# Optimization experiments

Measured on AMD Instinct MI355X. Metric: run time of the kernel, lower is better.

The kernel has to match this reference:

```python
import jax, jax.numpy as jnp
import numpy as np

N, E, G, NP = 65536, 524288, 256, 256
C, L, H, DH = 256, 4, 4, 64
IN_DIM, E_DIM = 771, 4
LN_EPS = 1e-5


def _ln(h, g, b):
    mu = jnp.mean(h, -1, keepdims=True)
    v = jnp.mean((h - mu) ** 2, -1, keepdims=True)
    return (h - mu) * jax.lax.rsqrt(v + LN_EPS) * g + b


def _bn(h, g, b):
    mu = jnp.mean(h, 0)
    v = jnp.mean((h - mu) ** 2, 0)
    return (h - mu) * jax.lax.rsqrt(v + LN_EPS) * g + b


def setup_inputs() -> dict:
    key = jax.random.key(0)
    ks = iter(jax.random.split(key, 64))
    def rn(shape, s=0.02):
        return jax.random.normal(next(ks), shape, jnp.float32) * s
    inp = {}
    inp["x"] = jax.random.normal(next(ks), (N, IN_DIM), jnp.float32)
    src = jax.random.randint(next(ks), (E,), 0, N, jnp.int32)
    dst = jax.random.randint(next(ks), (E,), 0, N, jnp.int32)
    inp["edge_index"] = jnp.stack([src, dst])
    inp["batch"] = jnp.arange(N, dtype=jnp.int32) // NP  # 256 graphs of 256 nodes
    inp["edge_attr"] = jax.random.normal(next(ks), (E, E_DIM), jnp.float32)
    # encoders
    inp["ne_w"] = rn((IN_DIM, C)); inp["ne_b"] = jnp.zeros((C,), jnp.float32)
    inp["ne_ln_g"] = jnp.ones((C,), jnp.float32); inp["ne_ln_b"] = jnp.zeros((C,), jnp.float32)
    inp["ee_w"] = rn((E_DIM, C)); inp["ee_b"] = jnp.zeros((C,), jnp.float32)
    # per-layer stacked params
    inp["eps"] = jnp.zeros((L,), jnp.float32)
    for nm, shape in [("elin_w", (L, C, C)), ("gin_w1", (L, C, C)), ("gin_w2", (L, C, C)),
                      ("attn_in_w", (L, 3 * C, C)), ("attn_out_w", (L, C, C)),
                      ("mlp_w1", (L, C, 2 * C)), ("mlp_w2", (L, 2 * C, C))]:
        inp[nm] = rn(shape)
    for nm, shape in [("elin_b", (L, C)), ("gin_b1", (L, C)), ("gin_b2", (L, C)),
                      ("attn_in_b", (L, 3 * C)), ("attn_out_b", (L, C)),
                      ("mlp_b1", (L, 2 * C)), ("mlp_b2", (L, C))]:
        inp[nm] = jnp.zeros(shape, jnp.float32)
    for nm in ["gin_bn_g", "ln1_g", "ln2_g", "ln3_g"]:
        inp[nm] = jnp.ones((L, C), jnp.float32)
    for nm in ["gin_bn_b", "ln1_b", "ln2_b", "ln3_b"]:
        inp[nm] = jnp.zeros((L, C), jnp.float32)
    inp["cls_w1"] = rn((C, C)); inp["cls_b1"] = jnp.zeros((C,), jnp.float32)
    inp["cls_ln_g"] = jnp.ones((C,), jnp.float32); inp["cls_ln_b"] = jnp.zeros((C,), jnp.float32)
    inp["cls_w2"] = rn((C, C // 2)); inp["cls_b2"] = jnp.zeros((C // 2,), jnp.float32)
    inp["cls_w3"] = rn((C // 2, 1)); inp["cls_b3"] = jnp.zeros((1,), jnp.float32)
    return inp


def _forward(edge_index, batch, x, edge_attr, ne_w, ne_b, ne_ln_g, ne_ln_b, ee_w, ee_b,
             eps, elin_w, elin_b, gin_w1, gin_b1, gin_bn_g, gin_bn_b, gin_w2, gin_b2,
             attn_in_w, attn_in_b, attn_out_w, attn_out_b,
             ln1_g, ln1_b, ln2_g, ln2_b, ln3_g, ln3_b,
             mlp_w1, mlp_b1, mlp_w2, mlp_b2,
             cls_w1, cls_b1, cls_ln_g, cls_ln_b, cls_w2, cls_b2, cls_w3, cls_b3):
    src, dst = edge_index[0], edge_index[1]
    # node / edge encoders (dropout = identity, eval mode)
    h = jax.nn.relu(_ln(x @ ne_w + ne_b, ne_ln_g, ne_ln_b))
    e = jax.nn.relu(edge_attr @ ee_w + ee_b)  # [E, C]
    scale = DH ** -0.5
    for l in range(L):
        # --- GINEConv: msg = relu(x_j + lin(edge_attr)), sum-aggregate at dst ---
        ee = e @ elin_w[l] + elin_b[l]
        msg = jax.nn.relu(h[src] + ee)                              # [E, C] gather
        aggr = jax.ops.segment_sum(msg, dst, num_segments=N)        # [N, C] scatter
        g1 = (1.0 + eps[l]) * h + aggr
        g1 = jax.nn.relu(_bn(g1 @ gin_w1[l] + gin_b1[l], gin_bn_g[l], gin_bn_b[l]))
        h_local = g1 @ gin_w2[l] + gin_b2[l]
        h_local = _ln(h_local + h, ln1_g[l], ln1_b[l])
        # --- global multi-head attention over dense-batched graphs ---
        hd = h.reshape(G, NP, C)
        qkv = hd @ attn_in_w[l].T + attn_in_b[l]                    # [G, NP, 3C]
        q, k, v = jnp.split(qkv, 3, axis=-1)
        q = q.reshape(G, NP, H, DH)
        k = k.reshape(G, NP, H, DH)
        v = v.reshape(G, NP, H, DH)
        scores = jnp.einsum('bqhd,bkhd->bhqk', q, k) * scale
        a = jax.nn.softmax(scores, axis=-1)
        o = jnp.einsum('bhqk,bkhd->bqhd', a, v).reshape(G, NP, C)
        o = (o @ attn_out_w[l].T + attn_out_b[l]).reshape(N, C)
        h_attn = _ln(o + h, ln2_g[l], ln2_b[l])
        # --- combine + FFN + final norm ---
        out = h_local + h_attn
        m = jax.nn.relu(out @ mlp_w1[l] + mlp_b1[l]) @ mlp_w2[l] + mlp_b2[l]
        h = _ln(out + m, ln3_g[l], ln3_b[l])
    # global mean pool per graph
    sums = jax.ops.segment_sum(h, batch, num_segments=G)
    cnt = jax.ops.segment_sum(jnp.ones((N, 1), h.dtype), batch, num_segments=G)
    gemb = sums / jnp.maximum(cnt, 1.0)
    z = jax.nn.relu(_ln(gemb @ cls_w1 + cls_b1, cls_ln_g, cls_ln_b))
    z = jax.nn.relu(z @ cls_w2 + cls_b2)
    return (z @ cls_w3 + cls_b3)[:, 0]


def reference(x, edge_index, batch, edge_attr, ne_w, ne_b, ne_ln_g, ne_ln_b, ee_w, ee_b,
              eps, elin_w, elin_b, gin_w1, gin_b1, gin_bn_g, gin_bn_b, gin_w2, gin_b2,
              attn_in_w, attn_in_b, attn_out_w, attn_out_b,
              ln1_g, ln1_b, ln2_g, ln2_b, ln3_g, ln3_b,
              mlp_w1, mlp_b1, mlp_w2, mlp_b2,
              cls_w1, cls_b1, cls_ln_g, cls_ln_b, cls_w2, cls_b2, cls_w3, cls_b3):
    return _forward(edge_index, batch, x, edge_attr, ne_w, ne_b, ne_ln_g, ne_ln_b, ee_w, ee_b,
                    eps, elin_w, elin_b, gin_w1, gin_b1, gin_bn_g, gin_bn_b, gin_w2, gin_b2,
                    attn_in_w, attn_in_b, attn_out_w, attn_out_b,
                    ln1_g, ln1_b, ln2_g, ln2_b, ln3_g, ln3_b,
                    mlp_w1, mlp_b1, mlp_w2, mlp_b2,
                    cls_w1, cls_b1, cls_ln_g, cls_ln_b, cls_w2, cls_b2, cls_w3, cls_b3)
```

## Files before the change

kernel.cpp:

```cpp
#include <hip/hip_runtime.h>
#include <hip/hip_bf16.h>
#include <math.h>

#define N_NODES 65536
#define N_EDGES 524288
#define CH 256

#define FMA4(A4, S, W4) \
  A4.x = fmaf((S), (W4).x, A4.x); A4.y = fmaf((S), (W4).y, A4.y); \
  A4.z = fmaf((S), (W4).z, A4.z); A4.w = fmaf((S), (W4).w, A4.w)

typedef __bf16 bf16x8 __attribute__((ext_vector_type(8)));
typedef float f32x4 __attribute__((ext_vector_type(4)));

__device__ inline unsigned short bf16rn(float v) {
  unsigned int u = __float_as_uint(v);
  u = u + 0x7FFFu + ((u >> 16) & 1u);
  return (unsigned short)(u >> 16);
}

__device__ inline bf16x8 pack_bf16_8(const float4 a, const float4 b) {
  union { __hip_bfloat162 h2[4]; bf16x8 v; } r;
  r.h2[0] = __float22bfloat162_rn(make_float2(a.x, a.y));
  r.h2[1] = __float22bfloat162_rn(make_float2(a.z, a.w));
  r.h2[2] = __float22bfloat162_rn(make_float2(b.x, b.y));
  r.h2[3] = __float22bfloat162_rn(make_float2(b.z, b.w));
  return r.v;
}

__global__ __launch_bounds__(256) void wcvt_kernel(
    const float* __restrict__ W, unsigned short* __restrict__ P,
    int K, int Nn, int transposed)
{
  const int idx = blockIdx.x * 256 + threadIdx.x;
  const int k = idx / Nn;
  const int n = idx - k * Nn;
  const float v = transposed ? W[(size_t)n * K + k] : W[(size_t)k * Nn + n];
  P[(((size_t)(k >> 3)) * Nn + n) * 8 + (k & 7)] = bf16rn(v);
}

__global__ __launch_bounds__(256) void xcvt_kernel(
    const float* __restrict__ x, unsigned short* __restrict__ xs)
{
  const int t = blockIdx.x * 256 + threadIdx.x;
  const int row = t / 98;
  const int c = t - row * 98;
  const int k0 = c << 3;
  unsigned short hi[8], lo[8];
#pragma unroll
  for (int j = 0; j < 8; ++j) {
    const int k = k0 + j;
    const float v = (k < 771) ? x[(size_t)row * 771 + k] : 0.f;
    const unsigned short h16 = bf16rn(v);
    const float hf = __uint_as_float(((unsigned int)h16) << 16);
    hi[j] = h16;
    lo[j] = bf16rn(v - hf);
  }
  unsigned short* base = xs + (size_t)row * 1568 + k0;
  *(uint4*)base = *(const uint4*)hi;
  *(uint4*)(base + 784) = *(const uint4*)lo;
}

template <bool RELU, bool ABF16>
__global__ __launch_bounds__(256, 3) void mgemm_kernel(
    const void* __restrict__ Av, const unsigned short* __restrict__ Bp,
    const float* __restrict__ bias, float* __restrict__ Cmat,
    int M, int Nn, int K)
{
  const int tid = threadIdx.x;
  const int lane = tid & 63;
  const int w = tid >> 6;
  const int m_base = blockIdx.y * 64;
  const int n_base = blockIdx.x * 256 + w * 64;
  const int lr = lane & 15;
  const int lq = lane >> 4;
  f32x4 acc[4][4];
#pragma unroll
  for (int i = 0; i < 4; ++i)
#pragma unroll
    for (int j = 0; j < 4; ++j) acc[i][j] = (f32x4){0.f, 0.f, 0.f, 0.f};

  for (int k0 = 0; k0 < K; k0 += 32) {
    const int ka = k0 + (lq << 3);
    bf16x8 af[4], bfv[4];
#pragma unroll
    for (int mt = 0; mt < 4; ++mt) {
      if (ABF16) {
        const unsigned short* ap =
            (const unsigned short*)Av + (size_t)(m_base + mt * 16 + lr) * K + ka;
        union { uint4 u; bf16x8 b; } au;
        au.u = *(const uint4*)ap;
        af[mt] = au.b;
      } else {
        const float* ap = (const float*)Av + (size_t)(m_base + mt * 16 + lr) * K + ka;
        af[mt] = pack_bf16_8(*(const float4*)ap, *(const float4*)(ap + 4));
      }
    }
#pragma unroll
    for (int nt = 0; nt < 4; ++nt) {
      const size_t off =
          (((size_t)(ka >> 3)) * Nn + (n_base + nt * 16 + lr)) << 3;
      union { uint4 u; bf16x8 b; } bu;
      bu.u = *(const uint4*)(Bp + off);
      bfv[nt] = bu.b;
    }
#pragma unroll
    for (int mt = 0; mt < 4; ++mt)
#pragma unroll
      for (int nt = 0; nt < 4; ++nt)
        acc[mt][nt] = __builtin_amdgcn_mfma_f32_16x16x32_bf16(
            af[mt], bfv[nt], acc[mt][nt], 0, 0, 0);
  }
#pragma unroll
  for (int nt = 0; nt < 4; ++nt) {
    const int col = n_base + nt * 16 + lr;
    const float bv = bias[col];
#pragma unroll
    for (int mt = 0; mt < 4; ++mt) {
      const int row0 = m_base + mt * 16 + (lq << 2);
#pragma unroll
      for (int r = 0; r < 4; ++r) {
        float v = acc[mt][nt][r] + bv;
        if (RELU) v = fmaxf(v, 0.f);
        Cmat[(size_t)(row0 + r) * Nn + col] = v;
      }
    }
  }
}

__global__ __launch_bounds__(256, 3) void eegemm_kernel(
    const float* __restrict__ edge_attr,
    const int* __restrict__ eid_sorted,
    const int* __restrict__ row_ptr, int node_base,
    const float* __restrict__ ee_w, const float* __restrict__ ee_b,
    const unsigned short* __restrict__ elin_p, const float* __restrict__ elin_b,
    float* __restrict__ EE)
{
  __shared__ float wenc[4][256];
  __shared__ float benc[256];
  const int tid = threadIdx.x;
  const int slot_base = row_ptr[node_base];
  const int slot_end = row_ptr[node_base + 16384];
  const int m_rel = blockIdx.y * 128;
  if (slot_base + m_rel >= slot_end) return;

  ((float4*)wenc)[tid] = ((const float4*)ee_w)[tid];
  if (tid < 64) ((float4*)benc)[tid] = ((const float4*)ee_b)[tid];
  __syncthreads();

  const int lane = tid & 63;
  const int w = tid >> 6;
  const int m_base = m_rel + (w >> 1) * 64;
  const int n_base = blockIdx.x * 128 + (w & 1) * 64;
  const int lr = lane & 15;
  const int lq = lane >> 4;

  float4 ea_r[4];
#pragma unroll
  for (int mt = 0; mt < 4; ++mt) {
    const int abs_slot = slot_base + m_base + mt * 16 + lr;
    if (abs_slot < slot_end) {
      const int e = eid_sorted[abs_slot];
      ea_r[mt] = *(const float4*)(edge_attr + ((size_t)e << 2));
    } else {
      ea_r[mt] = make_float4(0.f, 0.f, 0.f, 0.f);
    }
  }

  f32x4 acc[4][4];
#pragma unroll
  for (int i = 0; i < 4; ++i)
#pragma unroll
    for (int j = 0; j < 4; ++j) acc[i][j] = (f32x4){0.f, 0.f, 0.f, 0.f};

  for (int k0 = 0; k0 < 256; k0 += 32) {
    const int ka = k0 + (lq << 3);
    const float4 b0 = *(const float4*)&benc[ka];
    const float4 b1 = *(const float4*)&benc[ka + 4];
    float4 w0[4], w1[4];
#pragma unroll
    for (int j = 0; j < 4; ++j) {
      w0[j] = *(const float4*)&wenc[j][ka];
      w1[j] = *(const float4*)&wenc[j][ka + 4];
    }
    bf16x8 af[4], bfv[4];
#pragma unroll
    for (int mt = 0; mt < 4; ++mt) {
      float4 v0 = b0, v1 = b1;
      FMA4(v0, ea_r[mt].x, w0[0]); FMA4(v1, ea_r[mt].x, w1[0]);
      FMA4(v0, ea_r[mt].y, w0[1]); FMA4(v1, ea_r[mt].y, w1[1]);
      FMA4(v0, ea_r[mt].z, w0[2]); FMA4(v1, ea_r[mt].z, w1[2]);
      FMA4(v0, ea_r[mt].w, w0[3]); FMA4(v1, ea_r[mt].w, w1[3]);
      v0.x = fmaxf(v0.x, 0.f); v0.y = fmaxf(v0.y, 0.f);
      v0.z = fmaxf(v0.z, 0.f); v0.w = fmaxf(v0.w, 0.f);
      v1.x = fmaxf(v1.x, 0.f); v1.y = fmaxf(v1.y, 0.f);
      v1.z = fmaxf(v1.z, 0.f); v1.w = fmaxf(v1.w, 0.f);
      af[mt] = pack_bf16_8(v0, v1);
    }
#pragma unroll
    for (int nt = 0; nt < 4; ++nt) {
      const size_t off =
          (((size_t)(ka >> 3)) * 256 + (n_base + nt * 16 + lr)) << 3;
      union { uint4 u; bf16x8 b; } bu;
      bu.u = *(const uint4*)(elin_p + off);
      bfv[nt] = bu.b;
    }
#pragma unroll
    for (int mt = 0; mt < 4; ++mt)
#pragma unroll
      for (int nt = 0; nt < 4; ++nt)
        acc[mt][nt] = __builtin_amdgcn_mfma_f32_16x16x32_bf16(
            af[mt], bfv[nt], acc[mt][nt], 0, 0, 0);
  }

#pragma unroll
  for (int nt = 0; nt < 4; ++nt) {
    const int col = n_base + nt * 16 + lr;
    const float bv = elin_b[col];
#pragma unroll
    for (int mt = 0; mt < 4; ++mt) {
      const int row0 = m_base + mt * 16 + (lq << 2);
#pragma unroll
      for (int r = 0; r < 4; ++r) {
        if (slot_base + row0 + r < slot_end)
          EE[(size_t)(row0 + r) * 256 + col] = acc[mt][nt][r] + bv;
      }
    }
  }
}

__global__ __launch_bounds__(256, 8) void gscat2_kernel(
    const float* __restrict__ EE,
    const int* __restrict__ src_sorted,
    const int* __restrict__ row_ptr, int node_base,
    const float* __restrict__ h, const float* __restrict__ eps, int layer,
    float* __restrict__ g1)
{
  const int tid = threadIdx.x;
  const int w = tid >> 6;
  const int lane = tid & 63;
  const int n = node_base + (blockIdx.x << 2) + w;
  const int cg = lane << 2;
  const int slot_base = row_ptr[node_base];
  const int row_start = row_ptr[n];
  const int row_end = row_ptr[n + 1];

  float4 acc0 = make_float4(0.f, 0.f, 0.f, 0.f);
  float4 acc1 = make_float4(0.f, 0.f, 0.f, 0.f);
  int slot = row_start;
  for (; slot + 2 <= row_end; slot += 2) {
    const int s0 = src_sorted[slot];
    const int s1 = src_sorted[slot + 1];
    const float4 e0 = *(const float4*)(EE + (size_t)(slot - slot_base) * 256 + cg);
    const float4 e1 = *(const float4*)(EE + (size_t)(slot + 1 - slot_base) * 256 + cg);
    const float4 h0 = *(const float4*)(h + (((size_t)s0) << 8) + cg);
    const float4 h1 = *(const float4*)(h + (((size_t)s1) << 8) + cg);
    acc0.x += fmaxf(h0.x + e0.x, 0.f);
    acc0.y += fmaxf(h0.y + e0.y, 0.f);
    acc0.z += fmaxf(h0.z + e0.z, 0.f);
    acc0.w += fmaxf(h0.w + e0.w, 0.f);
    acc1.x += fmaxf(h1.x + e1.x, 0.f);
    acc1.y += fmaxf(h1.y + e1.y, 0.f);
    acc1.z += fmaxf(h1.z + e1.z, 0.f);
    acc1.w += fmaxf(h1.w + e1.w, 0.f);
  }
  if (slot < row_end) {
    const int s0 = src_sorted[slot];
    const float4 e0 = *(const float4*)(EE + (size_t)(slot - slot_base) * 256 + cg);
    const float4 h0 = *(const float4*)(h + (((size_t)s0) << 8) + cg);
    acc0.x += fmaxf(h0.x + e0.x, 0.f);
    acc0.y += fmaxf(h0.y + e0.y, 0.f);
    acc0.z += fmaxf(h0.z + e0.z, 0.f);
    acc0.w += fmaxf(h0.w + e0.w, 0.f);
  }
  acc0.x += acc1.x; acc0.y += acc1.y; acc0.z += acc1.z; acc0.w += acc1.w;

  const float f = 1.f + eps[layer];
  const float4 hv = *(const float4*)(h + (((size_t)n) << 8) + cg);
  float4 o;
  o.x = fmaf(f, hv.x, acc0.x);
  o.y = fmaf(f, hv.y, acc0.y);
  o.z = fmaf(f, hv.z, acc0.z);
  o.w = fmaf(f, hv.w, acc0.w);
  *(float4*)(g1 + (((size_t)n) << 8) + cg) = o;
}

template <bool BT, bool RELU>
__global__ __launch_bounds__(256, 4) void gemm_kernel(
    const float* __restrict__ A, const float* __restrict__ B,
    const float* __restrict__ bias, float* __restrict__ Cmat,
    int M, int Nn, int K)
{
  __shared__ float As[8][132];
  __shared__ float Bs[8][132];
  const int tid = threadIdx.x;
  const int bm = blockIdx.y * 128;
  const int bn = blockIdx.x * 128;
  const int tm = (tid >> 4) << 3;
  const int tn = (tid & 15) << 3;
  float acc[8][8];
#pragma unroll
  for (int i = 0; i < 8; ++i)
#pragma unroll
    for (int j = 0; j < 8; ++j) acc[i][j] = 0.f;

  const int nk = (K + 7) >> 3;
  const bool k4 = (K & 3) == 0;
  for (int kc = 0; kc < nk; ++kc) {
    const int k0 = kc << 3;
    {
      const int r = tid >> 1;
      const int kk = (tid & 1) << 2;
      const int gm = bm + r;
      float va[4] = {0.f, 0.f, 0.f, 0.f};
      if (gm < M) {
        const size_t base = (size_t)gm * K + k0 + kk;
        if (k4 && (k0 + kk + 4 <= K)) {
          const float4 v = *(const float4*)(A + base);
          va[0] = v.x; va[1] = v.y; va[2] = v.z; va[3] = v.w;
        } else {
#pragma unroll
          for (int j = 0; j < 4; ++j)
            if (k0 + kk + j < K) va[j] = A[base + j];
        }
      }
      As[kk + 0][r] = va[0]; As[kk + 1][r] = va[1];
      As[kk + 2][r] = va[2]; As[kk + 3][r] = va[3];
    }
    if (!BT) {
      const int r = tid >> 5;
      const int cb = (tid & 31) << 2;
      float4 v = make_float4(0.f, 0.f, 0.f, 0.f);
      if (k0 + r < K) v = *(const float4*)(B + (size_t)(k0 + r) * Nn + bn + cb);
      *(float4*)&Bs[r][cb] = v;
    } else {
      const int r = tid >> 1;
      const int kk = (tid & 1) << 2;
      float vb[4] = {0.f, 0.f, 0.f, 0.f};
      if (bn + r < Nn) {
        const size_t base = (size_t)(bn + r) * K + k0 + kk;
        if (k4 && (k0 + kk + 4 <= K)) {
          const float4 v = *(const float4*)(B + base);
          vb[0] = v.x; vb[1] = v.y; vb[2] = v.z; vb[3] = v.w;
        } else {
#pragma unroll
          for (int j = 0; j < 4; ++j)
            if (k0 + kk + j < K) vb[j] = B[base + j];
        }
      }
      Bs[kk + 0][r] = vb[0]; Bs[kk + 1][r] = vb[1];
      Bs[kk + 2][r] = vb[2]; Bs[kk + 3][r] = vb[3];
    }
    __syncthreads();
#pragma unroll
    for (int k = 0; k < 8; ++k) {
      const float4 a0 = *(const float4*)&As[k][tm];
      const float4 a1 = *(const float4*)&As[k][tm + 4];
      const float4 b0 = *(const float4*)&Bs[k][tn];
      const float4 b1 = *(const float4*)&Bs[k][tn + 4];
      const float av[8] = {a0.x, a0.y, a0.z, a0.w, a1.x, a1.y, a1.z, a1.w};
      const float bv[8] = {b0.x, b0.y, b0.z, b0.w, b1.x, b1.y, b1.z, b1.w};
#pragma unroll
      for (int i = 0; i < 8; ++i)
#pragma unroll
        for (int j = 0; j < 8; ++j)
          acc[i][j] = fmaf(av[i], bv[j], acc[i][j]);
    }
    __syncthreads();
  }
#pragma unroll
  for (int i = 0; i < 8; ++i) {
    const int gm = bm + tm + i;
    if (gm >= M) continue;
    float* crow = Cmat + (size_t)gm * Nn + bn + tn;
#pragma unroll
    for (int j = 0; j < 8; ++j) {
      const int gn = bn + tn + j;
      if (gn >= Nn) continue;
      float v = acc[i][j] + (bias ? bias[gn] : 0.f);
      if (RELU) v = fmaxf(v, 0.f);
      crow[j] = v;
    }
  }
}

__global__ __launch_bounds__(256) void hist_kernel(
    const int* __restrict__ dst, int* __restrict__ deg)
{
  const int e = blockIdx.x * 256 + threadIdx.x;
  atomicAdd(&deg[dst[e]], 1);
}

__global__ __launch_bounds__(256) void scan_kernel(
    const int* __restrict__ deg, int* __restrict__ row_ptr,
    int* __restrict__ fill)
{
  __shared__ int part[256];
  const int t = threadIdx.x;
  const int base = t << 8;
  int s = 0;
  for (int j = 0; j < 256; ++j) s += deg[base + j];
  part[t] = s;
  __syncthreads();
  for (int off = 1; off < 256; off <<= 1) {
    int v = (t >= off) ? part[t - off] : 0;
    __syncthreads();
    part[t] += v;
    __syncthreads();
  }
  int run = (t == 0) ? 0 : part[t - 1];
  for (int j = 0; j < 256; ++j) {
    row_ptr[base + j] = run;
    fill[base + j] = run;
    run += deg[base + j];
  }
  if (t == 255) row_ptr[65536] = run;
}

__global__ __launch_bounds__(256) void scatter_kernel(
    const int* __restrict__ dst, const int* __restrict__ src,
    int* __restrict__ fill, int* __restrict__ eid, int* __restrict__ ssrc)
{
  const int e = blockIdx.x * 256 + threadIdx.x;
  const int pos = atomicAdd(&fill[dst[e]], 1);
  eid[pos] = e;
  ssrc[pos] = src[e];
}

__global__ __launch_bounds__(256, 1) void mattn_kernel(
    const float* __restrict__ qkv, float* __restrict__ o)
{
  __shared__ __attribute__((aligned(16))) unsigned short Ks[256 * 72];
  __shared__ __attribute__((aligned(16))) unsigned short Vt[64 * 258];
  __shared__ __attribute__((aligned(16))) unsigned short Ps[4][64 * 72];
  const int tid = threadIdx.x;
  const int gh = blockIdx.x;
  const int g = gh >> 2;
  const int hh = gh & 3;
  const int lane = tid & 63;
  const int w = tid >> 6;
  const int lr = lane & 15;
  const int lq = lane >> 4;
  const float scale = 0.125f;

  {
    const int key0 = tid >> 4;
    const int c0 = (tid & 15) << 2;
#pragma unroll
    for (int it = 0; it < 16; ++it) {
      const int key = it * 16 + key0;
      const float* base = qkv + ((size_t)(g * 256 + key)) * 768 + hh * 64 + c0;
      const float4 kv = *(const float4*)(base + 256);
      const float4 vv = *(const float4*)(base + 512);
      union { __hip_bfloat162 h2[2]; ushort4 u; } pk;
      pk.h2[0] = __float22bfloat162_rn(make_float2(kv.x, kv.y));
      pk.h2[1] = __float22bfloat162_rn(make_float2(kv.z, kv.w));
      *(ushort4*)&Ks[key * 72 + c0] = pk.u;
      Vt[(c0 + 0) * 258 + key] = bf16rn(vv.x);
      Vt[(c0 + 1) * 258 + key] = bf16rn(vv.y);
      Vt[(c0 + 2) * 258 + key] = bf16rn(vv.z);
      Vt[(c0 + 3) * 258 + key] = bf16rn(vv.w);
    }
  }

  const int m0 = w * 64;
  bf16x8 qf[2][4];
#pragma unroll
  for (int ks = 0; ks < 2; ++ks)
#pragma unroll
    for (int mt = 0; mt < 4; ++mt) {
      const float* ap = qkv +
          ((size_t)(g * 256 + m0 + mt * 16 + lr)) * 768 + hh * 64 +
          ks * 32 + (lq << 3);
      float4 a = *(const float4*)ap;
      float4 b = *(const float4*)(ap + 4);
      a.x *= scale; a.y *= scale; a.z *= scale; a.w *= scale;
      b.x *= scale; b.y *= scale; b.z *= scale; b.w *= scale;
      qf[ks][mt] = pack_bf16_8(a, b);
    }
  __syncthreads();

  f32x4 oacc[4][4];
#pragma unroll
  for (int i = 0; i < 4; ++i)
#pragma unroll
    for (int j = 0; j < 4; ++j) oacc[i][j] = (f32x4){0.f, 0.f, 0.f, 0.f};
  float lpart[4][4];
#pragma unroll
  for (int i = 0; i < 4; ++i)
#pragma unroll
    for (int j = 0; j < 4; ++j) lpart[i][j] = 0.f;

  unsigned short* Pw = Ps[w];

  for (int kb = 0; kb < 4; ++kb) {
    f32x4 sacc[4][4];
#pragma unroll
    for (int i = 0; i < 4; ++i)
#pragma unroll
      for (int j = 0; j < 4; ++j) sacc[i][j] = (f32x4){0.f, 0.f, 0.f, 0.f};
#pragma unroll
    for (int ks = 0; ks < 2; ++ks) {
      bf16x8 bfv[4];
#pragma unroll
      for (int nt = 0; nt < 4; ++nt) {
        union { uint4 u; bf16x8 b; } bu;
        bu.u = *(const uint4*)&Ks[(kb * 64 + nt * 16 + lr) * 72 +
                                  ks * 32 + (lq << 3)];
        bfv[nt] = bu.b;
      }
#pragma unroll
      for (int mt = 0; mt < 4; ++mt)
#pragma unroll
        for (int nt = 0; nt < 4; ++nt)
          sacc[mt][nt] = __builtin_amdgcn_mfma_f32_16x16x32_bf16(
              qf[ks][mt], bfv[nt], sacc[mt][nt], 0, 0, 0);
    }
#pragma unroll
    for (int mt = 0; mt < 4; ++mt)
#pragma unroll
      for (int nt = 0; nt < 4; ++nt) {
#pragma unroll
        for (int rr = 0; rr < 4; ++rr) {
          const float p = __expf(sacc[mt][nt][rr]);
          lpart[mt][rr] += p;
          Pw[(mt * 16 + (lq << 2) + rr) * 72 + nt * 16 + lr] = bf16rn(p);
        }
      }
    asm volatile("s_waitcnt lgkmcnt(0)" ::: "memory");
    __builtin_amdgcn_sched_barrier(0);
#pragma unroll
    for (int ks = 0; ks < 2; ++ks) {
      bf16x8 pa[4], vb[4];
#pragma unroll
      for (int mt = 0; mt < 4; ++mt) {
        union { uint4 u; bf16x8 b; } au;
        au.u = *(const uint4*)&Pw[(mt * 16 + lr) * 72 + ks * 32 + (lq << 3)];
        pa[mt] = au.b;
      }
#pragma unroll
      for (int nt = 0; nt < 4; ++nt) {
        const unsigned short* vp =
            &Vt[(nt * 16 + lr) * 258 + kb * 64 + ks * 32 + (lq << 3)];
        union { unsigned int u4[4]; bf16x8 b; } vu;
        vu.u4[0] = *(const unsigned int*)(vp + 0);
        vu.u4[1] = *(const unsigned int*)(vp + 2);
        vu.u4[2] = *(const unsigned int*)(vp + 4);
        vu.u4[3] = *(const unsigned int*)(vp + 6);
        vb[nt] = vu.b;
      }
#pragma unroll
      for (int mt = 0; mt < 4; ++mt)
#pragma unroll
        for (int nt = 0; nt < 4; ++nt)
          oacc[mt][nt] = __builtin_amdgcn_mfma_f32_16x16x32_bf16(
              pa[mt], vb[nt], oacc[mt][nt], 0, 0, 0);
    }
  }

#pragma unroll
  for (int mt = 0; mt < 4; ++mt)
#pragma unroll
    for (int rr = 0; rr < 4; ++rr) {
      float v = lpart[mt][rr];
      v += __shfl_xor(v, 1);
      v += __shfl_xor(v, 2);
      v += __shfl_xor(v, 4);
      v += __shfl_xor(v, 8);
      lpart[mt][rr] = 1.f / v;
    }

#pragma unroll
  for (int mt = 0; mt < 4; ++mt) {
#pragma unroll
    for (int nt = 0; nt < 4; ++nt) {
#pragma unroll
      for (int rr = 0; rr < 4; ++rr) {
        const int row = m0 + mt * 16 + (lq << 2) + rr;
        o[((size_t)(g * 256 + row)) * 256 + hh * 64 + nt * 16 + lr] =
            oacc[mt][nt][rr] * lpart[mt][rr];
      }
    }
  }
}

__global__ __launch_bounds__(256) void ln_kernel(
    const float* __restrict__ a, const float* __restrict__ res,
    const float* __restrict__ gam, const float* __restrict__ bet,
    float* __restrict__ out, int relu)
{
  __shared__ float2 red[256];
  const int t = threadIdx.x;
  const size_t base = (size_t)blockIdx.x * 256;
  float v = a[base + t];
  if (res) v += res[base + t];
  red[t] = make_float2(v, v * v);
  __syncthreads();
#pragma unroll
  for (int s = 128; s > 0; s >>= 1) {
    if (t < s) { red[t].x += red[t + s].x; red[t].y += red[t + s].y; }
    __syncthreads();
  }
  const float mu = red[0].x * (1.f / 256.f);
  const float var = red[0].y * (1.f / 256.f) - mu * mu;
  float r = (v - mu) * rsqrtf(var + 1e-5f) * gam[t] + bet[t];
  if (relu) r = fmaxf(r, 0.f);
  out[base + t] = r;
}

__global__ __launch_bounds__(256) void bn_stats_kernel(
    const float* __restrict__ y, float* __restrict__ stats)
{
  const int t = threadIdx.x;
  const size_t r0 = (size_t)blockIdx.x * 64;
  float s = 0.f, s2 = 0.f;
  for (int r = 0; r < 64; ++r) {
    const float v = y[(r0 + r) * 256 + t];
    s += v;
    s2 = fmaf(v, v, s2);
  }
  atomicAdd(&stats[t], s);
  atomicAdd(&stats[256 + t], s2);
}

__global__ __launch_bounds__(256) void bn_apply_kernel(
    float* __restrict__ y, const float* __restrict__ stats,
    const float* __restrict__ gam, const float* __restrict__ bet)
{
  const size_t i = ((size_t)blockIdx.x * 256 + threadIdx.x) << 2;
  const int c = (int)(i & 255);
  const float inv_n = 1.f / 65536.f;
  float4 v = *(float4*)(y + i);
  const float4 s4 = *(const float4*)(stats + c);
  const float4 q4 = *(const float4*)(stats + 256 + c);
  const float4 g4 = *(const float4*)(gam + c);
  const float4 b4 = *(const float4*)(bet + c);
  float mu, var, sc;
  mu = s4.x * inv_n; var = q4.x * inv_n - mu * mu; sc = g4.x * rsqrtf(var + 1e-5f);
  v.x = fmaxf((v.x - mu) * sc + b4.x, 0.f);
  mu = s4.y * inv_n; var = q4.y * inv_n - mu * mu; sc = g4.y * rsqrtf(var + 1e-5f);
  v.y = fmaxf((v.y - mu) * sc + b4.y, 0.f);
  mu = s4.z * inv_n; var = q4.z * inv_n - mu * mu; sc = g4.z * rsqrtf(var + 1e-5f);
  v.z = fmaxf((v.z - mu) * sc + b4.z, 0.f);
  mu = s4.w * inv_n; var = q4.w * inv_n - mu * mu; sc = g4.w * rsqrtf(var + 1e-5f);
  v.w = fmaxf((v.w - mu) * sc + b4.w, 0.f);
  *(float4*)(y + i) = v;
}

__global__ __launch_bounds__(256) void add_kernel(
    const float* __restrict__ a, const float* __restrict__ b,
    float* __restrict__ out)
{
  const size_t i = ((size_t)blockIdx.x * 256 + threadIdx.x) << 2;
  const float4 va = *(const float4*)(a + i);
  const float4 vb = *(const float4*)(b + i);
  float4 v;
  v.x = va.x + vb.x; v.y = va.y + vb.y; v.z = va.z + vb.z; v.w = va.w + vb.w;
  *(float4*)(out + i) = v;
}

__global__ __launch_bounds__(256) void pool_kernel(
    const float* __restrict__ h, const int* __restrict__ batch,
    float* __restrict__ sums, float* __restrict__ cnt)
{
  const int t = threadIdx.x;
  const int n0 = blockIdx.x * 256;
  float acc = 0.f, runc = 0.f;
  int cur = batch[n0];
  for (int r = 0; r < 256; ++r) {
    const int n = n0 + r;
    const int b = batch[n];
    if (b != cur) {
      atomicAdd(&sums[(size_t)cur * 256 + t], acc);
      if (t == 0) atomicAdd(&cnt[cur], runc);
      acc = 0.f; runc = 0.f; cur = b;
    }
    acc += h[(size_t)n * 256 + t];
    runc += 1.f;
  }
  atomicAdd(&sums[(size_t)cur * 256 + t], acc);
  if (t == 0) atomicAdd(&cnt[cur], runc);
}

__global__ __launch_bounds__(256) void gemb_kernel(
    const float* __restrict__ sums, const float* __restrict__ cnt,
    float* __restrict__ gemb)
{
  const int i = blockIdx.x * 256 + threadIdx.x;
  const int g = i >> 8;
  gemb[i] = sums[i] / fmaxf(cnt[g], 1.f);
}

__global__ __launch_bounds__(256) void head_kernel(
    const float* __restrict__ z2, const float* __restrict__ w3,
    const float* __restrict__ b3, float* __restrict__ out)
{
  __shared__ float w[128];
  const int t = threadIdx.x;
  if (t < 128) w[t] = w3[t];
  __syncthreads();
  float s = 0.f;
  const float* row = z2 + (size_t)t * 128;
#pragma unroll 4
  for (int d = 0; d < 128; ++d) s = fmaf(row[d], w[d], s);
  out[t] = s + b3[0];
}

extern "C" void kernel_launch(void* const* d_in, const int* in_sizes, int n_in,
                              void* d_out, int out_size, void* d_ws, size_t ws_size,
                              hipStream_t stream)
{
  const float* x          = (const float*)d_in[0];
  const int*   edge_index = (const int*)d_in[1];
  const int*   batch      = (const int*)d_in[2];
  const float* edge_attr  = (const float*)d_in[3];
  const float* ne_w   = (const float*)d_in[4];
  const float* ne_b   = (const float*)d_in[5];
  const float* ne_ln_g = (const float*)d_in[6];
  const float* ne_ln_b = (const float*)d_in[7];
  const float* ee_w   = (const float*)d_in[8];
  const float* ee_b   = (const float*)d_in[9];
  const float* eps    = (const float*)d_in[10];
  const float* elin_w = (const float*)d_in[11];
  const float* gin_w1 = (const float*)d_in[12];
  const float* gin_w2 = (const float*)d_in[13];
  const float* attn_in_w  = (const float*)d_in[14];
  const float* attn_out_w = (const float*)d_in[15];
  const float* mlp_w1 = (const float*)d_in[16];
  const float* mlp_w2 = (const float*)d_in[17];
  const float* elin_b = (const float*)d_in[18];
  const float* gin_b1 = (const float*)d_in[19];
  const float* gin_b2 = (const float*)d_in[20];
  const float* attn_in_b  = (const float*)d_in[21];
  const float* attn_out_b = (const float*)d_in[22];
  const float* mlp_b1 = (const float*)d_in[23];
  const float* mlp_b2 = (const float*)d_in[24];
  const float* gin_bn_g = (const float*)d_in[25];
  const float* ln1_g  = (const float*)d_in[26];
  const float* ln2_g  = (const float*)d_in[27];
  const float* ln3_g  = (const float*)d_in[28];
  const float* gin_bn_b = (const float*)d_in[29];
  const float* ln1_b  = (const float*)d_in[30];
  const float* ln2_b  = (const float*)d_in[31];
  const float* ln3_b  = (const float*)d_in[32];
  const float* cls_w1 = (const float*)d_in[33];
  const float* cls_b1 = (const float*)d_in[34];
  const float* cls_ln_g = (const float*)d_in[35];
  const float* cls_ln_b = (const float*)d_in[36];
  const float* cls_w2 = (const float*)d_in[37];
  const float* cls_b2 = (const float*)d_in[38];
  const float* cls_w3 = (const float*)d_in[39];
  const float* cls_b3 = (const float*)d_in[40];

  const int* src = edge_index;
  const int* dst = edge_index + N_EDGES;

  float* ws = (float*)d_ws;
  const size_t NC = (size_t)N_NODES * CH;
  float* h    = ws;
  float* bufA = ws + NC;
  float* bufB = ws + 2 * NC;
  float* bufC = ws + 3 * NC;
  float* bufQ = ws + 4 * NC;
  float* stats = bufQ + (size_t)N_NODES * 768;
  int* ideg  = (int*)(stats + 2048);
  int* ifill = ideg + 65536;
  int* irow  = ifill + 65536;
  int* ieid  = irow + 65544;
  int* issrc = ieid + 524288;
  unsigned short* pan = (unsigned short*)(issrc + 524288);
  unsigned short* xs = (unsigned short*)bufC;
  float* sums = bufA;
  float* cnt  = bufA + 65536;
  float* gemb = bufA + 65792;
  float* z1   = bufA + 131328;
  float* z2   = bufA + 196864;

  const dim3 blk(256);
  const size_t PL = 720896;
  unsigned short* panNE = pan + 4 * PL;

  hipMemsetAsync(stats, 0, 2048 * sizeof(float), stream);
  hipMemsetAsync(ideg, 0, 65536 * sizeof(int), stream);
  hipMemsetAsync(panNE, 0, 401408 * sizeof(unsigned short), stream);
  hist_kernel<<<dim3(2048), blk, 0, stream>>>(dst, ideg);
  scan_kernel<<<dim3(1), blk, 0, stream>>>(ideg, irow, ifill);
  scatter_kernel<<<dim3(2048), blk, 0, stream>>>(dst, src, ifill, ieid, issrc);
  for (int l = 0; l < 4; ++l) {
    unsigned short* p = pan + l * PL;
    wcvt_kernel<<<dim3(256), blk, 0, stream>>>(gin_w1 + (size_t)l * 65536, p, 256, 256, 0);
    wcvt_kernel<<<dim3(256), blk, 0, stream>>>(gin_w2 + (size_t)l * 65536, p + 65536, 256, 256, 0);
    wcvt_kernel<<<dim3(768), blk, 0, stream>>>(attn_in_w + (size_t)l * 196608, p + 131072, 256, 768, 1);
    wcvt_kernel<<<dim3(256), blk, 0, stream>>>(attn_out_w + (size_t)l * 65536, p + 327680, 256, 256, 1);
    wcvt_kernel<<<dim3(512), blk, 0, stream>>>(mlp_w1 + (size_t)l * 131072, p + 393216, 256, 512, 0);
    wcvt_kernel<<<dim3(512), blk, 0, stream>>>(mlp_w2 + (size_t)l * 131072, p + 524288, 512, 256, 0);
    wcvt_kernel<<<dim3(256), blk, 0, stream>>>(elin_w + (size_t)l * 65536, p + 655360, 256, 256, 0);
  }
  wcvt_kernel<<<dim3(771), blk, 0, stream>>>(ne_w, panNE, 771, 256, 0);
  wcvt_kernel<<<dim3(771), blk, 0, stream>>>(ne_w, panNE + (size_t)98 * 256 * 8, 771, 256, 0);

  xcvt_kernel<<<dim3(25088), blk, 0, stream>>>(x, xs);
  mgemm_kernel<false, true><<<dim3(1, 1024), blk, 0, stream>>>(
      xs, panNE, ne_b, bufB, N_NODES, 256, 1568);
  ln_kernel<<<dim3(N_NODES), blk, 0, stream>>>(bufB, nullptr, ne_ln_g, ne_ln_b, h, 1);

  for (int l = 0; l < 4; ++l) {
    unsigned short* p = pan + l * PL;
    for (int q = 0; q < 4; ++q) {
      eegemm_kernel<<<dim3(2, 1056), blk, 0, stream>>>(
          edge_attr, ieid, irow, q * 16384, ee_w, ee_b,
          p + 655360, elin_b + l * 256, bufQ);
      gscat2_kernel<<<dim3(4096), blk, 0, stream>>>(
          bufQ, issrc, irow, q * 16384, h, eps, l, bufA);
    }
    mgemm_kernel<false, false><<<dim3(1, 1024), blk, 0, stream>>>(
        bufA, p, gin_b1 + l * 256, bufB, N_NODES, 256, 256);
    bn_stats_kernel<<<dim3(1024), blk, 0, stream>>>(bufB, stats + l * 512);
    bn_apply_kernel<<<dim3(16384), blk, 0, stream>>>(
        bufB, stats + l * 512, gin_bn_g + l * 256, gin_bn_b + l * 256);
    mgemm_kernel<false, false><<<dim3(1, 1024), blk, 0, stream>>>(
        bufB, p + 65536, gin_b2 + l * 256, bufC, N_NODES, 256, 256);
    ln_kernel<<<dim3(N_NODES), blk, 0, stream>>>(
        bufC, h, ln1_g + l * 256, ln1_b + l * 256, bufC, 0);
    mgemm_kernel<false, false><<<dim3(3, 1024), blk, 0, stream>>>(
        h, p + 131072, attn_in_b + l * 768, bufQ, N_NODES, 768, 256);
    mattn_kernel<<<dim3(1024), blk, 0, stream>>>(bufQ, bufA);
    mgemm_kernel<false, false><<<dim3(1, 1024), blk, 0, stream>>>(
        bufA, p + 327680, attn_out_b + l * 256, bufB, N_NODES, 256, 256);
    ln_kernel<<<dim3(N_NODES), blk, 0, stream>>>(
        bufB, h, ln2_g + l * 256, ln2_b + l * 256, bufB, 0);
    add_kernel<<<dim3(16384), blk, 0, stream>>>(bufC, bufB, bufB);
    mgemm_kernel<true, false><<<dim3(2, 1024), blk, 0, stream>>>(
        bufB, p + 393216, mlp_b1 + l * 512, bufQ, N_NODES, 512, 256);
    mgemm_kernel<false, false><<<dim3(1, 1024), blk, 0, stream>>>(
        bufQ, p + 524288, mlp_b2 + l * 256, bufC, N_NODES, 256, 512);
    ln_kernel<<<dim3(N_NODES), blk, 0, stream>>>(
        bufC, bufB, ln3_g + l * 256, ln3_b + l * 256, h, 0);
  }

  hipMemsetAsync(sums, 0, 65792 * sizeof(float), stream);
  pool_kernel<<<dim3(256), blk, 0, stream>>>(h, batch, sums, cnt);
  gemb_kernel<<<dim3(256), blk, 0, stream>>>(sums, cnt, gemb);
  gemm_kernel<false, false><<<dim3(2, 2), blk, 0, stream>>>(
      gemb, cls_w1, cls_b1, z1, 256, 256, 256);
  ln_kernel<<<dim3(256), blk, 0, stream>>>(z1, nullptr, cls_ln_g, cls_ln_b, z1, 1);
  gemm_kernel<false, true><<<dim3(1, 2), blk, 0, stream>>>(
      z1, cls_w2, cls_b2, z2, 256, 128, 256);
  head_kernel<<<dim3(1), blk, 0, stream>>>(z2, cls_w3, cls_b3, (float*)d_out);
}
```

Measured before the change: 6.040 ms.

## Store intermediate activations in bf16 to halve memory traffic across kernels

Producers (eegemm, gscat, bn_apply, add, LN, QKV and MLP1 GEMMs, attention output) now write bf16 copies of their outputs, and the matrix-core GEMMs and attention read these directly instead of converting fp32 inputs. This cuts bytes moved through HBM for the edge-embedding buffer, gather output, QKV and MLP hidden activations. The attention scale moves from Q to the exponent argument. The cost is extra rounding of intermediates, which may raise numerical error, and some LN/add kernels now do a second store.

```diff
diff --git a/kernel.cpp b/kernel.cpp
--- a/kernel.cpp
+++ b/kernel.cpp
@@ -17,6 +17,17 @@
   unsigned int u = __float_as_uint(v);
   u = u + 0x7FFFu + ((u >> 16) & 1u);
   return (unsigned short)(u >> 16);
+}
+
+__device__ inline float bf2f(unsigned short u) {
+  return __uint_as_float(((unsigned int)u) << 16);
+}
+
+__device__ inline ushort4 pack_bf16_4(const float4 a) {
+  ushort4 r;
+  r.x = bf16rn(a.x); r.y = bf16rn(a.y);
+  r.z = bf16rn(a.z); r.w = bf16rn(a.w);
+  return r;
 }
 
 __device__ inline bf16x8 pack_bf16_8(const float4 a, const float4 b) {
@@ -61,10 +72,10 @@
   *(uint4*)(base + 784) = *(const uint4*)lo;
 }
 
-template <bool RELU, bool ABF16>
+template <bool RELU, bool ABF16, bool CBF16>
 __global__ __launch_bounds__(256, 3) void mgemm_kernel(
     const void* __restrict__ Av, const unsigned short* __restrict__ Bp,
-    const float* __restrict__ bias, float* __restrict__ Cmat,
+    const float* __restrict__ bias, void* __restrict__ Cv,
     int M, int Nn, int K)
 {
   const int tid = threadIdx.x;
@@ -122,7 +133,10 @@
       for (int r = 0; r < 4; ++r) {
         float v = acc[mt][nt][r] + bv;
         if (RELU) v = fmaxf(v, 0.f);
-        Cmat[(size_t)(row0 + r) * Nn + col] = v;
+        if (CBF16)
+          ((unsigned short*)Cv)[(size_t)(row0 + r) * Nn + col] = bf16rn(v);
+        else
+          ((float*)Cv)[(size_t)(row0 + r) * Nn + col] = v;
       }
     }
   }
@@ -134,7 +148,7 @@
     const int* __restrict__ row_ptr, int node_base,
     const float* __restrict__ ee_w, const float* __restrict__ ee_b,
     const unsigned short* __restrict__ elin_p, const float* __restrict__ elin_b,
-    float* __restrict__ EE)
+    unsigned short* __restrict__ EE)
 {
   __shared__ float wenc[4][256];
   __shared__ float benc[256];
@@ -223,18 +237,18 @@
 #pragma unroll
       for (int r = 0; r < 4; ++r) {
         if (slot_base + row0 + r < slot_end)
-          EE[(size_t)(row0 + r) * 256 + col] = acc[mt][nt][r] + bv;
+          EE[(size_t)(row0 + r) * 256 + col] = bf16rn(acc[mt][nt][r] + bv);
       }
     }
   }
 }
 
 __global__ __launch_bounds__(256, 8) void gscat2_kernel(
-    const float* __restrict__ EE,
+    const unsigned short* __restrict__ EE,
     const int* __restrict__ src_sorted,
     const int* __restrict__ row_ptr, int node_base,
     const float* __restrict__ h, const float* __restrict__ eps, int layer,
-    float* __restrict__ g1)
+    unsigned short* __restrict__ g1b)
 {
   const int tid = threadIdx.x;
   const int w = tid >> 6;
@@ -251,27 +265,27 @@
   for (; slot + 2 <= row_end; slot += 2) {
     const int s0 = src_sorted[slot];
     const int s1 = src_sorted[slot + 1];
-    const float4 e0 = *(const float4*)(EE + (size_t)(slot - slot_base) * 256 + cg);
-    const float4 e1 = *(const float4*)(EE + (size_t)(slot + 1 - slot_base) * 256 + cg);
+    const ushort4 eu0 = *(const ushort4*)(EE + (size_t)(slot - slot_base) * 256 + cg);
+    const ushort4 eu1 = *(const ushort4*)(EE + (size_t)(slot + 1 - slot_base) * 256 + cg);
     const float4 h0 = *(const float4*)(h + (((size_t)s0) << 8) + cg);
     const float4 h1 = *(const float4*)(h + (((size_t)s1) << 8) + cg);
-    acc0.x += fmaxf(h0.x + e0.x, 0.f);
-    acc0.y += fmaxf(h0.y + e0.y, 0.f);
-    acc0.z += fmaxf(h0.z + e0.z, 0.f);
-    acc0.w += fmaxf(h0.w + e0.w, 0.f);
-    acc1.x += fmaxf(h1.x + e1.x, 0.f);
-    acc1.y += fmaxf(h1.y + e1.y, 0.f);
-    acc1.z += fmaxf(h1.z + e1.z, 0.f);
-    acc1.w += fmaxf(h1.w + e1.w, 0.f);
+    acc0.x += fmaxf(h0.x + bf2f(eu0.x), 0.f);
+    acc0.y += fmaxf(h0.y + bf2f(eu0.y), 0.f);
+    acc0.z += fmaxf(h0.z + bf2f(eu0.z), 0.f);
+    acc0.w += fmaxf(h0.w + bf2f(eu0.w), 0.f);
+    acc1.x += fmaxf(h1.x + bf2f(eu1.x), 0.f);
+    acc1.y += fmaxf(h1.y + bf2f(eu1.y), 0.f);
+    acc1.z += fmaxf(h1.z + bf2f(eu1.z), 0.f);
+    acc1.w += fmaxf(h1.w + bf2f(eu1.w), 0.f);
   }
   if (slot < row_end) {
     const int s0 = src_sorted[slot];
-    const float4 e0 = *(const float4*)(EE + (size_t)(slot - slot_base) * 256 + cg);
+    const ushort4 eu0 = *(const ushort4*)(EE + (size_t)(slot - slot_base) * 256 + cg);
     const float4 h0 = *(const float4*)(h + (((size_t)s0) << 8) + cg);
-    acc0.x += fmaxf(h0.x + e0.x, 0.f);
-    acc0.y += fmaxf(h0.y + e0.y, 0.f);
-    acc0.z += fmaxf(h0.z + e0.z, 0.f);
-    acc0.w += fmaxf(h0.w + e0.w, 0.f);
+    acc0.x += fmaxf(h0.x + bf2f(eu0.x), 0.f);
+    acc0.y += fmaxf(h0.y + bf2f(eu0.y), 0.f);
+    acc0.z += fmaxf(h0.z + bf2f(eu0.z), 0.f);
+    acc0.w += fmaxf(h0.w + bf2f(eu0.w), 0.f);
   }
   acc0.x += acc1.x; acc0.y += acc1.y; acc0.z += acc1.z; acc0.w += acc1.w;
 
@@ -282,7 +296,7 @@
   o.y = fmaf(f, hv.y, acc0.y);
   o.z = fmaf(f, hv.z, acc0.z);
   o.w = fmaf(f, hv.w, acc0.w);
-  *(float4*)(g1 + (((size_t)n) << 8) + cg) = o;
+  *(ushort4*)(g1b + (((size_t)n) << 8) + cg) = pack_bf16_4(o);
 }
 
 template <bool BT, bool RELU>
@@ -428,7 +442,7 @@
 }
 
 __global__ __launch_bounds__(256, 1) void mattn_kernel(
-    const float* __restrict__ qkv, float* __restrict__ o)
+    const unsigned short* __restrict__ qkv, unsigned short* __restrict__ o)
 {
   __shared__ __attribute__((aligned(16))) unsigned short Ks[256 * 72];
   __shared__ __attribute__((aligned(16))) unsigned short Vt[64 * 258];
@@ -441,7 +455,6 @@
   const int w = tid >> 6;
   const int lr = lane & 15;
   const int lq = lane >> 4;
-  const float scale = 0.125f;
 
   {
     const int key0 = tid >> 4;
@@ -449,17 +462,15 @@
 #pragma unroll
     for (int it = 0; it < 16; ++it) {
       const int key = it * 16 + key0;
-      const float* base = qkv + ((size_t)(g * 256 + key)) * 768 + hh * 64 + c0;
-      const float4 kv = *(const float4*)(base + 256);
-      const float4 vv = *(const float4*)(base + 512);
-      union { __hip_bfloat162 h2[2]; ushort4 u; } pk;
-      pk.h2[0] = __float22bfloat162_rn(make_float2(kv.x, kv.y));
-      pk.h2[1] = __float22bfloat162_rn(make_float2(kv.z, kv.w));
-      *(ushort4*)&Ks[key * 72 + c0] = pk.u;
-      Vt[(c0 + 0) * 258 + key] = bf16rn(vv.x);
-      Vt[(c0 + 1) * 258 + key] = bf16rn(vv.y);
-      Vt[(c0 + 2) * 258 + key] = bf16rn(vv.z);
-      Vt[(c0 + 3) * 258 + key] = bf16rn(vv.w);
+      const unsigned short* base =
+          qkv + ((size_t)(g * 256 + key)) * 768 + hh * 64 + c0;
+      const ushort4 kv = *(const ushort4*)(base + 256);
+      const ushort4 vv = *(const ushort4*)(base + 512);
+      *(ushort4*)&Ks[key * 72 + c0] = kv;
+      Vt[(c0 + 0) * 258 + key] = vv.x;
+      Vt[(c0 + 1) * 258 + key] = vv.y;
+      Vt[(c0 + 2) * 258 + key] = vv.z;
+      Vt[(c0 + 3) * 258 + key] = vv.w;
     }
   }
 
@@ -469,14 +480,12 @@
   for (int ks = 0; ks < 2; ++ks)
 #pragma unroll
     for (int mt = 0; mt < 4; ++mt) {
-      const float* ap = qkv +
+      const unsigned short* ap = qkv +
           ((size_t)(g * 256 + m0 + mt * 16 + lr)) * 768 + hh * 64 +
           ks * 32 + (lq << 3);
-      float4 a = *(const float4*)ap;
-      float4 b = *(const float4*)(ap + 4);
-      a.x *= scale; a.y *= scale; a.z *= scale; a.w *= scale;
-      b.x *= scale; b.y *= scale; b.z *= scale; b.w *= scale;
-      qf[ks][mt] = pack_bf16_8(a, b);
+      union { uint4 u; bf16x8 b; } au;
+      au.u = *(const uint4*)ap;
+      qf[ks][mt] = au.b;
     }
   __syncthreads();
 
@@ -522,7 +531,7 @@
       for (int nt = 0; nt < 4; ++nt) {
 #pragma unroll
         for (int rr = 0; rr < 4; ++rr) {
-          const float p = __expf(sacc[mt][nt][rr]);
+          const float p = __expf(sacc[mt][nt][rr] * 0.125f);
           lpart[mt][rr] += p;
           Pw[(mt * 16 + (lq << 2) + rr) * 72 + nt * 16 + lr] = bf16rn(p);
         }
@@ -578,7 +587,7 @@
       for (int rr = 0; rr < 4; ++rr) {
         const int row = m0 + mt * 16 + (lq << 2) + rr;
         o[((size_t)(g * 256 + row)) * 256 + hh * 64 + nt * 16 + lr] =
-            oacc[mt][nt][rr] * lpart[mt][rr];
+            bf16rn(oacc[mt][nt][rr] * lpart[mt][rr]);
       }
     }
   }
@@ -587,7 +596,7 @@
 __global__ __launch_bounds__(256) void ln_kernel(
     const float* __restrict__ a, const float* __restrict__ res,
     const float* __restrict__ gam, const float* __restrict__ bet,
-    float* __restrict__ out, int relu)
+    float* __restrict__ out, int relu, unsigned short* __restrict__ outb)
 {
   __shared__ float2 red[256];
   const int t = threadIdx.x;
@@ -606,6 +615,7 @@
   float r = (v - mu) * rsqrtf(var + 1e-5f) * gam[t] + bet[t];
   if (relu) r = fmaxf(r, 0.f);
   out[base + t] = r;
+  if (outb) outb[base + t] = bf16rn(r);
 }
 
 __global__ __launch_bounds__(256) void bn_stats_kernel(
@@ -624,13 +634,14 @@
 }
 
 __global__ __launch_bounds__(256) void bn_apply_kernel(
-    float* __restrict__ y, const float* __restrict__ stats,
-    const float* __restrict__ gam, const float* __restrict__ bet)
+    const float* __restrict__ y, const float* __restrict__ stats,
+    const float* __restrict__ gam, const float* __restrict__ bet,
+    unsigned short* __restrict__ yb)
 {
   const size_t i = ((size_t)blockIdx.x * 256 + threadIdx.x) << 2;
   const int c = (int)(i & 255);
   const float inv_n = 1.f / 65536.f;
-  float4 v = *(float4*)(y + i);
+  float4 v = *(const float4*)(y + i);
   const float4 s4 = *(const float4*)(stats + c);
   const float4 q4 = *(const float4*)(stats + 256 + c);
   const float4 g4 = *(const float4*)(gam + c);
@@ -644,12 +655,12 @@
   v.z = fmaxf((v.z - mu) * sc + b4.z, 0.f);
   mu = s4.w * inv_n; var = q4.w * inv_n - mu * mu; sc = g4.w * rsqrtf(var + 1e-5f);
   v.w = fmaxf((v.w - mu) * sc + b4.w, 0.f);
-  *(float4*)(y + i) = v;
+  *(ushort4*)(yb + i) = pack_bf16_4(v);
 }
 
 __global__ __launch_bounds__(256) void add_kernel(
     const float* __restrict__ a, const float* __restrict__ b,
-    float* __restrict__ out)
+    float* __restrict__ out, unsigned short* __restrict__ outb)
 {
   const size_t i = ((size_t)blockIdx.x * 256 + threadIdx.x) << 2;
   const float4 va = *(const float4*)(a + i);
@@ -657,6 +668,7 @@
   float4 v;
   v.x = va.x + vb.x; v.y = va.y + vb.y; v.z = va.z + vb.z; v.w = va.w + vb.w;
   *(float4*)(out + i) = v;
+  *(ushort4*)(outb + i) = pack_bf16_4(v);
 }
 
 __global__ __launch_bounds__(256) void pool_kernel(
@@ -769,6 +781,11 @@
   int* ieid  = irow + 65544;
   int* issrc = ieid + 524288;
   unsigned short* pan = (unsigned short*)(issrc + 524288);
+  unsigned short* abuf = (unsigned short*)bufA;
+  unsigned short* EEb  = (unsigned short*)bufQ;
+  unsigned short* qkvb = (unsigned short*)bufQ;
+  unsigned short* m1b  = (unsigned short*)bufQ;
+  unsigned short* hb   = (unsigned short*)(bufQ + (size_t)24 * 1024 * 1024);
   unsigned short* xs = (unsigned short*)bufC;
   float* sums = bufA;
   float* cnt  = bufA + 65536;
@@ -800,42 +817,42 @@
   wcvt_kernel<<<dim3(771), blk, 0, stream>>>(ne_w, panNE + (size_t)98 * 256 * 8, 771, 256, 0);
 
   xcvt_kernel<<<dim3(25088), blk, 0, stream>>>(x, xs);
-  mgemm_kernel<false, true><<<dim3(1, 1024), blk, 0, stream>>>(
+  mgemm_kernel<false, true, false><<<dim3(1, 1024), blk, 0, stream>>>(
       xs, panNE, ne_b, bufB, N_NODES, 256, 1568);
-  ln_kernel<<<dim3(N_NODES), blk, 0, stream>>>(bufB, nullptr, ne_ln_g, ne_ln_b, h, 1);
+  ln_kernel<<<dim3(N_NODES), blk, 0, stream>>>(bufB, nullptr, ne_ln_g, ne_ln_b, h, 1, hb);
 
   for (int l = 0; l < 4; ++l) {
     unsigned short* p = pan + l * PL;
     for (int q = 0; q < 4; ++q) {
       eegemm_kernel<<<dim3(2, 1056), blk, 0, stream>>>(
           edge_attr, ieid, irow, q * 16384, ee_w, ee_b,
-          p + 655360, elin_b + l * 256, bufQ);
+          p + 655360, elin_b + l * 256, EEb);
       gscat2_kernel<<<dim3(4096), blk, 0, stream>>>(
-          bufQ, issrc, irow, q * 16384, h, eps, l, bufA);
-    }
-    mgemm_kernel<false, false><<<dim3(1, 1024), blk, 0, stream>>>(
-        bufA, p, gin_b1 + l * 256, bufB, N_NODES, 256, 256);
+          EEb, issrc, irow, q * 16384, h, eps, l, abuf);
+    }
+    mgemm_kernel<false, true, false><<<dim3(1, 1024), blk, 0, stream>>>(
+        abuf, p, gin_b1 + l * 256, bufB, N_NODES, 256, 256);
     bn_stats_kernel<<<dim3(1024), blk, 0, stream>>>(bufB, stats + l * 512);
     bn_apply_kernel<<<dim3(16384), blk, 0, stream>>>(
-        bufB, stats + l * 512, gin_bn_g + l * 256, gin_bn_b + l * 256);
-    mgemm_kernel<false, false><<<dim3(1, 1024), blk, 0, stream>>>(
-        bufB, p + 65536, gin_b2 + l * 256, bufC, N_NODES, 256, 256);
+        bufB, stats + l * 512, gin_bn_g + l * 256, gin_bn_b + l * 256, abuf);
+    mgemm_kernel<false, true, false><<<dim3(1, 1024), blk, 0, stream>>>(
+        abuf, p + 65536, gin_b2 + l * 256, bufC, N_NODES, 256, 256);
     ln_kernel<<<dim3(N_NODES), blk, 0, stream>>>(
-        bufC, h, ln1_g + l * 256, ln1_b + l * 256, bufC, 0);
-    mgemm_kernel<false, false><<<dim3(3, 1024), blk, 0, stream>>>(
-        h, p + 131072, attn_in_b + l * 768, bufQ, N_NODES, 768, 256);
-    mattn_kernel<<<dim3(1024), blk, 0, stream>>>(bufQ, bufA);
-    mgemm_kernel<false, false><<<dim3(1, 1024), blk, 0, stream>>>(
-        bufA, p + 327680, attn_out_b + l * 256, bufB, N_NODES, 256, 256);
+        bufC, h, ln1_g + l * 256, ln1_b + l * 256, bufC, 0, nullptr);
+    mgemm_kernel<false, true, true><<<dim3(3, 1024), blk, 0, stream>>>(
+        hb, p + 131072, attn_in_b + l * 768, qkvb, N_NODES, 768, 256);
+    mattn_kernel<<<dim3(1024), blk, 0, stream>>>(qkvb, abuf);
+    mgemm_kernel<false, true, false><<<dim3(1, 1024), blk, 0, stream>>>(
+        abuf, p + 327680, attn_out_b + l * 256, bufB, N_NODES, 256, 256);
     ln_kernel<<<dim3(N_NODES), blk, 0, stream>>>(
-        bufB, h, ln2_g + l * 256, ln2_b + l * 256, bufB, 0);
-    add_kernel<<<dim3(16384), blk, 0, stream>>>(bufC, bufB, bufB);
-    mgemm_kernel<true, false><<<dim3(2, 1024), blk, 0, stream>>>(
-        bufB, p + 393216, mlp_b1 + l * 512, bufQ, N_NODES, 512, 256);
-    mgemm_kernel<false, false><<<dim3(1, 1024), blk, 0, stream>>>(
-        bufQ, p + 524288, mlp_b2 + l * 256, bufC, N_NODES, 256, 512);
+        bufB, h, ln2_g + l * 256, ln2_b + l * 256, bufB, 0, nullptr);
+    add_kernel<<<dim3(16384), blk, 0, stream>>>(bufC, bufB, bufB, abuf);
+    mgemm_kernel<true, true, true><<<dim3(2, 1024), blk, 0, stream>>>(
+        abuf, p + 393216, mlp_b1 + l * 512, m1b, N_NODES, 512, 256);
+    mgemm_kernel<false, true, false><<<dim3(1, 1024), blk, 0, stream>>>(
+        m1b, p + 524288, mlp_b2 + l * 256, bufC, N_NODES, 256, 512);
     ln_kernel<<<dim3(N_NODES), blk, 0, stream>>>(
-        bufC, bufB, ln3_g + l * 256, ln3_b + l * 256, h, 0);
+        bufC, bufB, ln3_g + l * 256, ln3_b + l * 256, h, 0, hb);
   }
 
   hipMemsetAsync(sums, 0, 65792 * sizeof(float), stream);
@@ -843,7 +860,7 @@
   gemb_kernel<<<dim3(256), blk, 0, stream>>>(sums, cnt, gemb);
   gemm_kernel<false, false><<<dim3(2, 2), blk, 0, stream>>>(
       gemb, cls_w1, cls_b1, z1, 256, 256, 256);
-  ln_kernel<<<dim3(256), blk, 0, stream>>>(z1, nullptr, cls_ln_g, cls_ln_b, z1, 1);
+  ln_kernel<<<dim3(256), blk, 0, stream>>>(z1, nullptr, cls_ln_g, cls_ln_b, z1, 1, nullptr);
   gemm_kernel<false, true><<<dim3(1, 2), blk, 0, stream>>>(
       z1, cls_w2, cls_b2, z2, 256, 128, 256);
   head_kernel<<<dim3(1), blk, 0, stream>>>(z2, cls_w3, cls_b3, (float*)d_out);
```

Result: faster. 5.063 ms (-16.2%).
